# Performance work log

Measured on AMD Instinct MI355X. Metric: run time of the kernel, lower is better.

The kernel has to match this reference:

```python
import jax, jax.numpy as jnp
import numpy as np

DIM = 1024
HEADS = 16
HEAD_DIM = DIM // HEADS


def setup_inputs() -> dict:
    key = jax.random.key(0)
    ks = jax.random.split(key, 7)
    scale = 1.0 / np.sqrt(DIM)
    x = jax.random.normal(ks[0], (2, 2048, DIM), dtype=jnp.float32)
    Wq = jax.random.uniform(ks[1], (DIM, DIM), jnp.float32, -scale, scale)
    bq = jax.random.uniform(ks[2], (DIM,), jnp.float32, -scale, scale)
    Wk = jax.random.uniform(ks[3], (DIM, DIM), jnp.float32, -scale, scale)
    bk = jax.random.uniform(ks[4], (DIM,), jnp.float32, -scale, scale)
    Wv = jax.random.uniform(ks[5], (DIM, DIM), jnp.float32, -scale, scale)
    bv = jax.random.uniform(ks[6], (DIM,), jnp.float32, -scale, scale)
    return {"x": x, "Wq": Wq, "bq": bq, "Wk": Wk, "bk": bk, "Wv": Wv, "bv": bv}


def reference(x, Wq, bq, Wk, bk, Wv, bv):
    b, s, _ = x.shape
    # torch Linear: y = x @ W.T + b
    q = (x @ Wq.T + bq).reshape(b, s, HEADS, HEAD_DIM)
    k = (x @ Wk.T + bk).reshape(b, s, HEADS, HEAD_DIM)
    v = (x @ Wv.T + bv).reshape(b, s, HEADS, HEAD_DIM)
    # scores: (b, s, z, h), softmax over z (key axis = axis 2)
    scores = jnp.einsum('bshd,bzhd->bszh', q, k) / jnp.sqrt(jnp.float32(HEAD_DIM))
    attention = jax.nn.softmax(scores, axis=2)
    output = jnp.einsum('bzhd,bszh->bshd', v, attention)
    return output
```

## Files before the change

### kernel.cpp

```cpp
#include <hip/hip_runtime.h>

typedef unsigned short u16;
typedef __attribute__((ext_vector_type(8))) __bf16 bf16x8;
typedef __attribute__((ext_vector_type(4))) float f32x4;
typedef __attribute__((ext_vector_type(8))) u16 u16x8;

#define BATCH 2
#define SEQ   2048
#define DIM   1024
#define HEADS 16
#define HDIM  64

#define QSCALE 0.18033688011112042f

__device__ __forceinline__ float bf2f(u16 u) {
  union { unsigned int u; float f; } v; v.u = ((unsigned int)u) << 16; return v.f;
}
__device__ __forceinline__ u16 f2bf(float f) {
  union { float f; unsigned int u; } v; v.f = f;
  unsigned int r = v.u + 0x7fffu + ((v.u >> 16) & 1u);
  return (u16)(r >> 16);
}

__device__ __forceinline__ void async16(u16* lds, const u16* g) {
  __builtin_amdgcn_global_load_lds(
      (__attribute__((address_space(1))) void*)(void*)(g),
      (__attribute__((address_space(3))) void*)(lds), 16, 0, 0);
}

#define XG  524288
#define WG  131072
extern "C" __global__ __launch_bounds__(256)
void convert_all(const float* __restrict__ x,  const float* __restrict__ wq,
                 const float* __restrict__ wk, const float* __restrict__ wv,
                 u16* __restrict__ xbf, u16* __restrict__ wbf)
{
  const int g = blockIdx.x * 256 + threadIdx.x;
  const float* src; u16* dst; size_t off;
  if (g < XG)               { src = x;  dst = xbf;                 off = (size_t)g; }
  else if (g < XG + WG)     { src = wq; dst = wbf;                 off = (size_t)(g - XG); }
  else if (g < XG + 2 * WG) { src = wk; dst = wbf + DIM * DIM;     off = (size_t)(g - XG - WG); }
  else                      { src = wv; dst = wbf + 2 * DIM * DIM; off = (size_t)(g - XG - 2 * WG); }
  f32x4 a = *(const f32x4*)(src + off * 8);
  f32x4 b = *(const f32x4*)(src + off * 8 + 4);
  u16x8 o;
#pragma unroll
  for (int i = 0; i < 4; ++i) { o[i] = f2bf(a[i]); o[4 + i] = f2bf(b[i]); }
  *(u16x8*)(dst + off * 8) = o;
}

extern "C" __global__ __launch_bounds__(256)
void qkv_gemm(const u16* __restrict__ xbf, const u16* __restrict__ wbf,
              const float* __restrict__ bq, const float* __restrict__ bk,
              const float* __restrict__ bv,
              u16* __restrict__ qo, u16* __restrict__ ko, u16* __restrict__ vto)
{
  __shared__ alignas(16) u16 Albs[128 * 32];
  __shared__ alignas(16) u16 Blbs[128 * 32];

  const int which = blockIdx.z;
  const u16* Wb = wbf + (size_t)which * DIM * DIM;
  const float* bias = (which == 0) ? bq : (which == 1) ? bk : bv;

  const int lane = threadIdx.x & 63;
  const int wave = threadIdx.x >> 6;
  const int l16  = lane & 15;
  const int quad = lane >> 4;
  const int lrow = lane >> 2;
  const int lcol = (lane & 3) * 8;

  const int mBase = blockIdx.y * 128;
  const int nBase = blockIdx.x * 128;
  const int mw = (wave >> 1) * 64;
  const int nw = (wave & 1) * 64;

  f32x4 acc[4][4] = {};

  for (int k0 = 0; k0 < DIM; k0 += 32) {
#pragma unroll
    for (int p = 0; p < 2; ++p) {
      const int r16 = wave * 2 + p;
      const int row = r16 * 16 + lrow;
      async16(&Albs[r16 * 512], xbf + (size_t)(mBase + row) * DIM + k0 + lcol);
      async16(&Blbs[r16 * 512], Wb  + (size_t)(nBase + row) * DIM + k0 + lcol);
    }
    asm volatile("s_waitcnt vmcnt(0)" ::: "memory");
    __syncthreads();

    bf16x8 af[4], bfr[4];
#pragma unroll
    for (int i = 0; i < 4; ++i) {
      af[i]  = *(const bf16x8*)&Albs[(mw + i * 16 + l16) * 32 + quad * 8];
      bfr[i] = *(const bf16x8*)&Blbs[(nw + i * 16 + l16) * 32 + quad * 8];
    }
#pragma unroll
    for (int mi = 0; mi < 4; ++mi)
#pragma unroll
      for (int ni = 0; ni < 4; ++ni)
        acc[mi][ni] = __builtin_amdgcn_mfma_f32_16x16x32_bf16(af[mi], bfr[ni], acc[mi][ni], 0, 0, 0);
    __syncthreads();
  }

  const float oscale = (which == 0) ? QSCALE : 1.0f;
#pragma unroll
  for (int ni = 0; ni < 4; ++ni) {
    const int n = nBase + nw + ni * 16 + l16;
    const float bval = bias[n];
    const int h = n >> 6, d = n & 63;
#pragma unroll
    for (int mi = 0; mi < 4; ++mi) {
#pragma unroll
      for (int r = 0; r < 4; ++r) {
        const int m = mBase + mw + mi * 16 + quad * 4 + r;
        const int bi = m >> 11, s = m & 2047;
        const u16 val = f2bf((acc[mi][ni][r] + bval) * oscale);
        if (which == 2) {
          vto[((size_t)(bi * HEADS + h) * HDIM + d) * SEQ + s] = val;
        } else {
          u16* dst = (which == 0) ? qo : ko;
          dst[((size_t)(bi * HEADS + h) * SEQ + s) * HDIM + d] = val;
        }
      }
    }
  }
}

extern "C" __global__ __launch_bounds__(256)
void attn(const u16* __restrict__ q, const u16* __restrict__ k,
          const u16* __restrict__ vt, float* __restrict__ out)
{
  __shared__ alignas(16) u16 Klds[2][64 * 64];
  __shared__ alignas(16) u16 Vlds[2][64 * 64];
  __shared__ alignas(16) u16 Plds[4][16 * 64];

  const int lane = threadIdx.x & 63;
  const int wave = threadIdx.x >> 6;
  const int l16  = lane & 15;
  const int quad = lane >> 4;
  const int r8   = lane >> 3;
  const int sl   = lane & 7;
  const int jsw  = sl ^ (r8 & 7);

  const int h  = blockIdx.y;
  const int b  = blockIdx.z;
  const int q0 = blockIdx.x * 64 + wave * 16;

  const u16* qh  = q  + (size_t)(b * HEADS + h) * SEQ * HDIM;
  const u16* kh  = k  + (size_t)(b * HEADS + h) * SEQ * HDIM;
  const u16* vth = vt + (size_t)(b * HEADS + h) * HDIM * SEQ;

  bf16x8 qf[2];
#pragma unroll
  for (int ks = 0; ks < 2; ++ks)
    qf[ks] = *(const bf16x8*)(qh + (size_t)(q0 + l16) * HDIM + ks * 32 + quad * 8);

  float lsum[4] = {};
  f32x4 o[4] = {};
  u16* pw = &Plds[wave][0];

#pragma unroll
  for (int p = 0; p < 2; ++p) {
    const int i = wave * 2 + p;
    async16(&Klds[0][i * 512], kh + (size_t)(i * 8 + r8) * HDIM + jsw * 8);
    async16(&Vlds[0][i * 512], vth + (size_t)(i * 8 + r8) * SEQ + jsw * 8);
  }

  for (int it = 0; it < 32; ++it) {
    const int bb = it & 1;
    if (it < 31) {
      __syncthreads();
      const int kb1 = (it + 1) * 64;
#pragma unroll
      for (int p = 0; p < 2; ++p) {
        const int i = wave * 2 + p;
        async16(&Klds[bb ^ 1][i * 512], kh + (size_t)(kb1 + i * 8 + r8) * HDIM + jsw * 8);
        async16(&Vlds[bb ^ 1][i * 512], vth + (size_t)(i * 8 + r8) * SEQ + kb1 + jsw * 8);
      }
      asm volatile("s_waitcnt vmcnt(4)" ::: "memory");
    } else {
      asm volatile("s_waitcnt vmcnt(0)" ::: "memory");
    }
    __syncthreads();

    const u16* Kb = &Klds[bb][0];
    const u16* Vb = &Vlds[bb][0];

    f32x4 sc[4] = {};
#pragma unroll
    for (int ks = 0; ks < 2; ++ks) {
      const int sw = (((ks * 4 + quad) ^ (l16 & 7)) * 8);
#pragma unroll
      for (int nt = 0; nt < 4; ++nt) {
        bf16x8 kf = *(const bf16x8*)&Kb[(nt * 16 + l16) * 64 + sw];
        sc[nt] = __builtin_amdgcn_mfma_f32_16x16x32_bf16(qf[ks], kf, sc[nt], 0, 0, 0);
      }
    }

#pragma unroll
    for (int r = 0; r < 4; ++r) {
      const int prow = quad * 4 + r;
      const int rx = (quad & 1) * 4 + r;
#pragma unroll
      for (int nt = 0; nt < 4; ++nt) {
        const float p = __builtin_exp2f(sc[nt][r]);
        lsum[r] += p;
        const int c = nt * 2 + (l16 >> 3);
        pw[prow * 64 + ((c ^ rx) * 8) + (l16 & 7)] = f2bf(p);
      }
    }

#pragma unroll
    for (int ks = 0; ks < 2; ++ks) {
      const int sw = (((ks * 4 + quad) ^ (l16 & 7)) * 8);
      bf16x8 pf = *(const bf16x8*)&pw[l16 * 64 + sw];
#pragma unroll
      for (int dt = 0; dt < 4; ++dt) {
        bf16x8 vfr = *(const bf16x8*)&Vb[(dt * 16 + l16) * 64 + sw];
        o[dt] = __builtin_amdgcn_mfma_f32_16x16x32_bf16(pf, vfr, o[dt], 0, 0, 0);
      }
    }
  }

#pragma unroll
  for (int r = 0; r < 4; ++r) {
#pragma unroll
    for (int off = 1; off < 16; off <<= 1)
      lsum[r] += __shfl_xor(lsum[r], off, 64);
    const float inv = 1.f / fmaxf(lsum[r], 1e-20f);
    const int s = q0 + quad * 4 + r;
#pragma unroll
    for (int dt = 0; dt < 4; ++dt) {
      const int d = dt * 16 + l16;
      out[((size_t)(b * SEQ + s) * HEADS + h) * HDIM + d] = o[dt][r] * inv;
    }
  }
}

extern "C" void kernel_launch(void* const* d_in, const int* in_sizes, int n_in,
                              void* d_out, int out_size, void* d_ws, size_t ws_size,
                              hipStream_t stream) {
  (void)in_sizes; (void)n_in; (void)out_size; (void)ws_size;
  const float* x  = (const float*)d_in[0];
  const float* Wq = (const float*)d_in[1];
  const float* bq = (const float*)d_in[2];
  const float* Wk = (const float*)d_in[3];
  const float* bk = (const float*)d_in[4];
  const float* Wv = (const float*)d_in[5];
  const float* bv = (const float*)d_in[6];
  float* out = (float*)d_out;

  u16* ws = (u16*)d_ws;
  const size_t XSZ = (size_t)BATCH * SEQ * DIM;
  const size_t WSZ = (size_t)DIM * DIM;
  const size_t QSZ = (size_t)BATCH * HEADS * SEQ * HDIM;
  u16* xbf   = ws;
  u16* wbf   = ws + XSZ;
  u16* qbuf  = ws + XSZ + 3 * WSZ;
  u16* kbuf  = qbuf + QSZ;
  u16* vtbuf = kbuf + QSZ;

  convert_all<<<3584, 256, 0, stream>>>(x, Wq, Wk, Wv, xbf, wbf);

  dim3 g1(DIM / 128, (BATCH * SEQ) / 128, 3);
  qkv_gemm<<<g1, 256, 0, stream>>>(xbf, wbf, bq, bk, bv, qbuf, kbuf, vtbuf);

  dim3 g2(SEQ / 64, HEADS, BATCH);
  attn<<<g2, 256, 0, stream>>>(qbuf, kbuf, vtbuf, out);
}
```

Measured before the change: 196.8 us.

## Double-buffer QKV GEMM loads and give each attention wave two query tiles

The QKV GEMM now uses double-buffered LDS tiles, so the next K-slice loads while the current one is computed, and one barrier per iteration is removed. The attention kernel processes 32 queries per wave instead of 16, reusing each K and V fragment read from LDS for two MFMA tiles and halving the grid. The scores MFMA operands are swapped (K times Q) so P can be written as packed bf16 pairs and row sums reduced with fewer shuffles. This costs more registers and LDS, which may reduce occupancy, and halves the number of attention blocks.

```diff
diff --git a/kernel.cpp b/kernel.cpp
--- a/kernel.cpp
+++ b/kernel.cpp
@@ -1,4 +1,5 @@
 #include <hip/hip_runtime.h>
+#include <hip/hip_bf16.h>
 
 typedef unsigned short u16;
 typedef __attribute__((ext_vector_type(8))) __bf16 bf16x8;
@@ -20,6 +21,11 @@
   union { float f; unsigned int u; } v; v.f = f;
   unsigned int r = v.u + 0x7fffu + ((v.u >> 16) & 1u);
   return (u16)(r >> 16);
+}
+__device__ __forceinline__ unsigned int pk2(float a, float b) {
+  union { __hip_bfloat162 h2; unsigned int u; } v;
+  v.h2 = __float22bfloat162_rn(float2{a, b});
+  return v.u;
 }
 
 __device__ __forceinline__ void async16(u16* lds, const u16* g) {
@@ -55,8 +61,8 @@
               const float* __restrict__ bv,
               u16* __restrict__ qo, u16* __restrict__ ko, u16* __restrict__ vto)
 {
-  __shared__ alignas(16) u16 Albs[128 * 32];
-  __shared__ alignas(16) u16 Blbs[128 * 32];
+  __shared__ alignas(16) u16 Albs[2][128 * 32];
+  __shared__ alignas(16) u16 Blbs[2][128 * 32];
 
   const int which = blockIdx.z;
   const u16* Wb = wbf + (size_t)which * DIM * DIM;
@@ -76,29 +82,43 @@
 
   f32x4 acc[4][4] = {};
 
-  for (int k0 = 0; k0 < DIM; k0 += 32) {
-#pragma unroll
-    for (int p = 0; p < 2; ++p) {
-      const int r16 = wave * 2 + p;
-      const int row = r16 * 16 + lrow;
-      async16(&Albs[r16 * 512], xbf + (size_t)(mBase + row) * DIM + k0 + lcol);
-      async16(&Blbs[r16 * 512], Wb  + (size_t)(nBase + row) * DIM + k0 + lcol);
-    }
-    asm volatile("s_waitcnt vmcnt(0)" ::: "memory");
+#pragma unroll
+  for (int p = 0; p < 2; ++p) {
+    const int r16 = wave * 2 + p;
+    const int row = r16 * 16 + lrow;
+    async16(&Albs[0][r16 * 512], xbf + (size_t)(mBase + row) * DIM + lcol);
+    async16(&Blbs[0][r16 * 512], Wb  + (size_t)(nBase + row) * DIM + lcol);
+  }
+
+  for (int it = 0; it < 32; ++it) {
+    const int bb = it & 1;
+    if (it < 31) {
+      __syncthreads();
+      const int k0n = (it + 1) * 32;
+#pragma unroll
+      for (int p = 0; p < 2; ++p) {
+        const int r16 = wave * 2 + p;
+        const int row = r16 * 16 + lrow;
+        async16(&Albs[bb ^ 1][r16 * 512], xbf + (size_t)(mBase + row) * DIM + k0n + lcol);
+        async16(&Blbs[bb ^ 1][r16 * 512], Wb  + (size_t)(nBase + row) * DIM + k0n + lcol);
+      }
+      asm volatile("s_waitcnt vmcnt(4)" ::: "memory");
+    } else {
+      asm volatile("s_waitcnt vmcnt(0)" ::: "memory");
+    }
     __syncthreads();
 
     bf16x8 af[4], bfr[4];
 #pragma unroll
     for (int i = 0; i < 4; ++i) {
-      af[i]  = *(const bf16x8*)&Albs[(mw + i * 16 + l16) * 32 + quad * 8];
-      bfr[i] = *(const bf16x8*)&Blbs[(nw + i * 16 + l16) * 32 + quad * 8];
+      af[i]  = *(const bf16x8*)&Albs[bb][(mw + i * 16 + l16) * 32 + quad * 8];
+      bfr[i] = *(const bf16x8*)&Blbs[bb][(nw + i * 16 + l16) * 32 + quad * 8];
     }
 #pragma unroll
     for (int mi = 0; mi < 4; ++mi)
 #pragma unroll
       for (int ni = 0; ni < 4; ++ni)
         acc[mi][ni] = __builtin_amdgcn_mfma_f32_16x16x32_bf16(af[mi], bfr[ni], acc[mi][ni], 0, 0, 0);
-    __syncthreads();
   }
 
   const float oscale = (which == 0) ? QSCALE : 1.0f;
@@ -131,7 +151,7 @@
 {
   __shared__ alignas(16) u16 Klds[2][64 * 64];
   __shared__ alignas(16) u16 Vlds[2][64 * 64];
-  __shared__ alignas(16) u16 Plds[4][16 * 64];
+  __shared__ alignas(16) u16 Plds[4][32 * 64];
 
   const int lane = threadIdx.x & 63;
   const int wave = threadIdx.x >> 6;
@@ -140,28 +160,31 @@
   const int r8   = lane >> 3;
   const int sl   = lane & 7;
   const int jsw  = sl ^ (r8 & 7);
-
-  const int h  = blockIdx.y;
-  const int b  = blockIdx.z;
-  const int q0 = blockIdx.x * 64 + wave * 16;
+  const int e7   = l16 & 7;
+
+  const int h     = blockIdx.y;
+  const int b     = blockIdx.z;
+  const int qbase = blockIdx.x * 128 + wave * 32;
 
   const u16* qh  = q  + (size_t)(b * HEADS + h) * SEQ * HDIM;
   const u16* kh  = k  + (size_t)(b * HEADS + h) * SEQ * HDIM;
   const u16* vth = vt + (size_t)(b * HEADS + h) * HDIM * SEQ;
 
-  bf16x8 qf[2];
-#pragma unroll
-  for (int ks = 0; ks < 2; ++ks)
-    qf[ks] = *(const bf16x8*)(qh + (size_t)(q0 + l16) * HDIM + ks * 32 + quad * 8);
-
-  float lsum[4] = {};
-  f32x4 o[4] = {};
+  bf16x8 qf[2][2];
+#pragma unroll
+  for (int qg = 0; qg < 2; ++qg)
+#pragma unroll
+    for (int ks = 0; ks < 2; ++ks)
+      qf[qg][ks] = *(const bf16x8*)(qh + (size_t)(qbase + qg * 16 + l16) * HDIM + ks * 32 + quad * 8);
+
+  float lsum[2] = {};
+  f32x4 o[2][4] = {};
   u16* pw = &Plds[wave][0];
 
 #pragma unroll
   for (int p = 0; p < 2; ++p) {
     const int i = wave * 2 + p;
-    async16(&Klds[0][i * 512], kh + (size_t)(i * 8 + r8) * HDIM + jsw * 8);
+    async16(&Klds[0][i * 512], kh  + (size_t)(i * 8 + r8) * HDIM + jsw * 8);
     async16(&Vlds[0][i * 512], vth + (size_t)(i * 8 + r8) * SEQ + jsw * 8);
   }
 
@@ -173,7 +196,7 @@
 #pragma unroll
       for (int p = 0; p < 2; ++p) {
         const int i = wave * 2 + p;
-        async16(&Klds[bb ^ 1][i * 512], kh + (size_t)(kb1 + i * 8 + r8) * HDIM + jsw * 8);
+        async16(&Klds[bb ^ 1][i * 512], kh  + (size_t)(kb1 + i * 8 + r8) * HDIM + jsw * 8);
         async16(&Vlds[bb ^ 1][i * 512], vth + (size_t)(i * 8 + r8) * SEQ + kb1 + jsw * 8);
       }
       asm volatile("s_waitcnt vmcnt(4)" ::: "memory");
@@ -185,53 +208,69 @@
     const u16* Kb = &Klds[bb][0];
     const u16* Vb = &Vlds[bb][0];
 
-    f32x4 sc[4] = {};
+    f32x4 sc[2][4] = {};
 #pragma unroll
     for (int ks = 0; ks < 2; ++ks) {
-      const int sw = (((ks * 4 + quad) ^ (l16 & 7)) * 8);
 #pragma unroll
       for (int nt = 0; nt < 4; ++nt) {
-        bf16x8 kf = *(const bf16x8*)&Kb[(nt * 16 + l16) * 64 + sw];
-        sc[nt] = __builtin_amdgcn_mfma_f32_16x16x32_bf16(qf[ks], kf, sc[nt], 0, 0, 0);
-      }
-    }
-
+        bf16x8 kf = *(const bf16x8*)&Kb[(nt * 16 + l16) * 64 + ((ks * 4 + quad) ^ e7) * 8];
+#pragma unroll
+        for (int qg = 0; qg < 2; ++qg)
+          sc[qg][nt] = __builtin_amdgcn_mfma_f32_16x16x32_bf16(kf, qf[qg][ks], sc[qg][nt], 0, 0, 0);
+      }
+    }
+
+#pragma unroll
+    for (int qg = 0; qg < 2; ++qg) {
+      float ls = 0.f;
+#pragma unroll
+      for (int nt = 0; nt < 4; ++nt) {
+        const float p0 = __builtin_exp2f(sc[qg][nt][0]);
+        const float p1 = __builtin_exp2f(sc[qg][nt][1]);
+        const float p2 = __builtin_exp2f(sc[qg][nt][2]);
+        const float p3 = __builtin_exp2f(sc[qg][nt][3]);
+        ls += (p0 + p1) + (p2 + p3);
+        uint2 pkv; pkv.x = pk2(p0, p1); pkv.y = pk2(p2, p3);
+        *(uint2*)(pw + (qg * 16 + l16) * 64
+                  + ((nt * 2 + (quad >> 1)) ^ e7) * 8 + (quad & 1) * 4) = pkv;
+      }
+      lsum[qg] += ls;
+    }
+
+#pragma unroll
+    for (int ks = 0; ks < 2; ++ks) {
+      bf16x8 pf0 = *(const bf16x8*)&pw[(0 * 16 + l16) * 64 + ((ks * 4 + quad) ^ e7) * 8];
+      bf16x8 pf1 = *(const bf16x8*)&pw[(1 * 16 + l16) * 64 + ((ks * 4 + quad) ^ e7) * 8];
+#pragma unroll
+      for (int dt = 0; dt < 4; ++dt) {
+        bf16x8 vfr = *(const bf16x8*)&Vb[(dt * 16 + l16) * 64 + ((ks * 4 + quad) ^ e7) * 8];
+        o[0][dt] = __builtin_amdgcn_mfma_f32_16x16x32_bf16(pf0, vfr, o[0][dt], 0, 0, 0);
+        o[1][dt] = __builtin_amdgcn_mfma_f32_16x16x32_bf16(pf1, vfr, o[1][dt], 0, 0, 0);
+      }
+    }
+  }
+
+#pragma unroll
+  for (int qg = 0; qg < 2; ++qg) {
+    lsum[qg] += __shfl_xor(lsum[qg], 16, 64);
+    lsum[qg] += __shfl_xor(lsum[qg], 32, 64);
+  }
+  asm volatile("s_waitcnt lgkmcnt(0)" ::: "memory");
+  float* lw = (float*)pw;
+  if (lane < 16) { lw[lane] = lsum[0]; lw[16 + lane] = lsum[1]; }
+  asm volatile("s_waitcnt lgkmcnt(0)" ::: "memory");
+
+#pragma unroll
+  for (int qg = 0; qg < 2; ++qg) {
 #pragma unroll
     for (int r = 0; r < 4; ++r) {
-      const int prow = quad * 4 + r;
-      const int rx = (quad & 1) * 4 + r;
-#pragma unroll
-      for (int nt = 0; nt < 4; ++nt) {
-        const float p = __builtin_exp2f(sc[nt][r]);
-        lsum[r] += p;
-        const int c = nt * 2 + (l16 >> 3);
-        pw[prow * 64 + ((c ^ rx) * 8) + (l16 & 7)] = f2bf(p);
-      }
-    }
-
-#pragma unroll
-    for (int ks = 0; ks < 2; ++ks) {
-      const int sw = (((ks * 4 + quad) ^ (l16 & 7)) * 8);
-      bf16x8 pf = *(const bf16x8*)&pw[l16 * 64 + sw];
+      const float inv = 1.f / fmaxf(lw[qg * 16 + quad * 4 + r], 1e-20f);
+      const int s = qbase + qg * 16 + quad * 4 + r;
 #pragma unroll
       for (int dt = 0; dt < 4; ++dt) {
-        bf16x8 vfr = *(const bf16x8*)&Vb[(dt * 16 + l16) * 64 + sw];
-        o[dt] = __builtin_amdgcn_mfma_f32_16x16x32_bf16(pf, vfr, o[dt], 0, 0, 0);
-      }
-    }
-  }
-
-#pragma unroll
-  for (int r = 0; r < 4; ++r) {
-#pragma unroll
-    for (int off = 1; off < 16; off <<= 1)
-      lsum[r] += __shfl_xor(lsum[r], off, 64);
-    const float inv = 1.f / fmaxf(lsum[r], 1e-20f);
-    const int s = q0 + quad * 4 + r;
-#pragma unroll
-    for (int dt = 0; dt < 4; ++dt) {
-      const int d = dt * 16 + l16;
-      out[((size_t)(b * SEQ + s) * HEADS + h) * HDIM + d] = o[dt][r] * inv;
+        const int d = dt * 16 + l16;
+        out[((size_t)(b * SEQ + s) * HEADS + h) * HDIM + d] = o[qg][dt][r] * inv;
+      }
     }
   }
 }
@@ -264,6 +303,6 @@
   dim3 g1(DIM / 128, (BATCH * SEQ) / 128, 3);
   qkv_gemm<<<g1, 256, 0, stream>>>(xbf, wbf, bq, bk, bv, qbuf, kbuf, vtbuf);
 
-  dim3 g2(SEQ / 64, HEADS, BATCH);
+  dim3 g2(SEQ / 128, HEADS, BATCH);
   attn<<<g2, 256, 0, stream>>>(qbuf, kbuf, vtbuf, out);
 }
```

After: 200.0 us. Within noise of the previous version (+1.6%).
